# Performance work log

Measured on AMD Instinct MI355X. Metric: run time of the kernel, lower is better.

Reference implementation:

```python
import jax, jax.numpy as jnp
import numpy as np

B, HW, N = 32, 4096, 16
E, KV, FFN = 256, 256, 1024
NUM_ITER = 3
EPS_LN = 1e-5
EPS_ATTN = 1e-5


def _ln(x, g, b):
    m = x.mean(-1, keepdims=True)
    v = ((x - m) ** 2).mean(-1, keepdims=True)
    return (x - m) / jnp.sqrt(v + EPS_LN) * g + b


def _gru_cell(x, h, w_ih, w_hh, b_ih, b_hh):
    # PyTorch GRUCell semantics; gate order r, z, n
    gi = x @ w_ih.T + b_ih
    gh = h @ w_hh.T + b_hh
    ir, iz, inn = jnp.split(gi, 3, axis=-1)
    hr, hz, hn = jnp.split(gh, 3, axis=-1)
    r = jax.nn.sigmoid(ir + hr)
    z = jax.nn.sigmoid(iz + hz)
    n = jnp.tanh(inn + r * hn)
    return (1.0 - z) * n + z * h


def setup_inputs() -> dict:
    key = jax.random.key(0)
    ks = jax.random.split(key, 16)
    s = 0.02
    return {
        "input": jax.random.normal(ks[0], (B, HW, KV), jnp.float32),
        "query": jax.random.normal(ks[1], (B, N, E), jnp.float32),
        "g_kv": jnp.ones((KV,), jnp.float32),
        "b_kv": jnp.zeros((KV,), jnp.float32),
        "w_k": jax.random.normal(ks[2], (E, KV), jnp.float32) * s,
        "w_v": jax.random.normal(ks[3], (E, KV), jnp.float32) * s,
        "g_q": jnp.ones((E,), jnp.float32),
        "b_q": jnp.zeros((E,), jnp.float32),
        "w_q": jax.random.normal(ks[4], (E, E), jnp.float32) * s,
        "w_ih": jax.random.normal(ks[5], (3 * E, E), jnp.float32) * s,
        "w_hh": jax.random.normal(ks[6], (3 * E, E), jnp.float32) * s,
        "b_ih": jnp.zeros((3 * E,), jnp.float32),
        "b_hh": jnp.zeros((3 * E,), jnp.float32),
        "g_2": jnp.ones((E,), jnp.float32),
        "b_2": jnp.zeros((E,), jnp.float32),
        "w_f1": jax.random.normal(ks[7], (FFN, E), jnp.float32) * s,
        "b_f1": jnp.zeros((FFN,), jnp.float32),
        "w_f2": jax.random.normal(ks[8], (E, FFN), jnp.float32) * s,
        "b_f2": jnp.zeros((E,), jnp.float32),
    }


def reference(input, query, g_kv, b_kv, w_k, w_v, g_q, b_q, w_q,
              w_ih, w_hh, b_ih, b_hh, g_2, b_2, w_f1, b_f1, w_f2, b_f2):
    b, n, e = query.shape
    kv = _ln(input, g_kv, b_kv)              # (b, hw, kv)
    k = kv @ w_k.T                           # (b, hw, e)
    v = kv @ w_v.T                           # (b, hw, e)
    scale = e ** (-0.5)

    q = query
    attn = None
    for i in range(NUM_ITER):
        if i + 1 == NUM_ITER:  # bi-level truncated backprop
            q = jax.lax.stop_gradient(q) + query - jax.lax.stop_gradient(query)
        slots_prev = q
        qn = _ln(q, g_q, b_q)
        qp = (qn @ w_q.T) * scale            # (b, n, e)
        logit = jnp.einsum("bqc,bkc->bqk", qp, k)
        attn = jax.nn.softmax(logit, axis=1)           # softmax over slots (inverted)
        attn_w = attn / (attn.sum(2, keepdims=True) + EPS_ATTN)
        updates = jnp.einsum("bqk,bkc->bqc", attn_w, v)
        slots = _gru_cell(updates.reshape(b * n, e), slots_prev.reshape(b * n, e),
                          w_ih, w_hh, b_ih, b_hh).reshape(b, n, e)
        h = jax.nn.gelu(_ln(slots, g_2, b_2) @ w_f1.T + b_f1)
        q = slots + h @ w_f2.T + b_f2
    return q, attn
```

## Files before the change

kernel.cpp:

```cpp
#include <hip/hip_runtime.h>
#include <math.h>

#define NB 32
#define HW 4096
#define NS 16
#define EDIM 256
#define FFND 1024
#define EPS_LN 1e-5f
#define EPS_ATTN 1e-5f
#define BPB 32
#define RPB 128
#define TROWS 16

__device__ __forceinline__ float sigmoidf_(float x) { return 1.0f / (1.0f + __expf(-x)); }
__device__ __forceinline__ float gelu_(float x) {
    float x3 = x * x * x;
    return 0.5f * x * (1.0f + tanhf(0.7978845608028654f * (x + 0.044715f * x3)));
}

__global__ void k_prep(const float* __restrict__ w_q, const float* __restrict__ w_k,
                       float* __restrict__ W) {
    const int j = blockIdx.x;
    const int c = threadIdx.x;
    float acc = 0.f;
    for (int e = 0; e < EDIM; ++e)
        acc += w_q[e * EDIM + j] * w_k[e * EDIM + c];
    W[j * EDIM + c] = acc * 0.0625f;
}

__global__ __launch_bounds__(256) void k_tr(const float* __restrict__ src,
                                            float* __restrict__ dst, int R, int C) {
    __shared__ float tile[64][65];
    const int tilesC = C >> 6;
    const int tR = (blockIdx.x / tilesC) << 6;
    const int tC = (blockIdx.x % tilesC) << 6;
    const int t = threadIdx.x;
    {
        const int r = t >> 2;
        const int c0 = (t & 3) << 4;
#pragma unroll
        for (int i = 0; i < 16; i += 4) {
            const float4 v = *reinterpret_cast<const float4*>(src + (size_t)(tR + r) * C + tC + c0 + i);
            tile[r][c0 + i] = v.x; tile[r][c0 + i + 1] = v.y;
            tile[r][c0 + i + 2] = v.z; tile[r][c0 + i + 3] = v.w;
        }
    }
    __syncthreads();
    {
        const int c = t >> 2;
        const int r0 = (t & 3) << 4;
#pragma unroll
        for (int i = 0; i < 16; ++i)
            dst[(size_t)(tC + c) * R + tR + r0 + i] = tile[r0 + i][c];
    }
}

__global__ void k_qproj(const float* __restrict__ qsrc, const float* __restrict__ g_q,
                        const float* __restrict__ b_q, const float* __restrict__ W,
                        const float* __restrict__ g_kv, const float* __restrict__ b_kv,
                        float* __restrict__ qpk, float* __restrict__ gqbq) {
    const int row = blockIdx.x;
    const int t = threadIdx.x;
    __shared__ float qn[EDIM];
    __shared__ float red[16];
    const float v = qsrc[(size_t)row * EDIM + t];
    float s = v, ss = v * v;
#pragma unroll
    for (int m = 1; m < 64; m <<= 1) { s += __shfl_xor(s, m); ss += __shfl_xor(ss, m); }
    const int wave = t >> 6, lane = t & 63;
    if (lane == 0) { red[wave] = s; red[8 + wave] = ss; }
    __syncthreads();
    const float st = red[0] + red[1] + red[2] + red[3];
    const float sst = red[8] + red[9] + red[10] + red[11];
    const float mean = st * (1.0f / EDIM);
    const float rstd = rsqrtf(sst * (1.0f / EDIM) - mean * mean + EPS_LN);
    qn[t] = (v - mean) * rstd * g_q[t] + b_q[t];
    __syncthreads();
    float acc = 0.f;
    for (int j = 0; j < EDIM; ++j)
        acc += qn[j] * W[j * EDIM + t];
    qpk[(size_t)row * EDIM + t] = acc;
    float u = acc * g_kv[t];
    float w2 = acc * b_kv[t];
#pragma unroll
    for (int m = 1; m < 64; m <<= 1) { u += __shfl_xor(u, m); w2 += __shfl_xor(w2, m); }
    __syncthreads();
    if (lane == 0) { red[wave] = u; red[8 + wave] = w2; }
    __syncthreads();
    if (t == 0) {
        const int b = row >> 4, sl = row & 15;
        gqbq[b * 32 + sl] = red[0] + red[1] + red[2] + red[3];
        gqbq[b * 32 + 16 + sl] = red[8] + red[9] + red[10] + red[11];
    }
}

template <bool LAST>
__global__ __launch_bounds__(256, 2) void k_bigpass(
    const float* __restrict__ input, const float* __restrict__ qpk,
    const float* __restrict__ gqbq, const float* __restrict__ g_kv,
    float* __restrict__ pacc, float* __restrict__ psum, float* __restrict__ attn_out) {
    const int b = blockIdx.x >> 5;
    const int sub = blockIdx.x & 31;
    const int t = threadIdx.x;
    const int w = t >> 6;
    const int lane = t & 63;
    const int g = t >> 4;
    const int j = t & 15;

    __shared__ __align__(16) float G[NS][EDIM];
    __shared__ __align__(16) float stage[TROWS][264];
    __shared__ __align__(16) float wrec[TROWS][20];
    __shared__ float gqbq_s[2][NS];

#pragma unroll
    for (int i = 0; i < 4; ++i) {
        const int idx = i * 1024 + t * 4;
        const float4 qv = *reinterpret_cast<const float4*>(qpk + (size_t)b * 4096 + idx);
        const float4 gv = *reinterpret_cast<const float4*>(g_kv + (idx & 255));
        *reinterpret_cast<float4*>(&G[0][0] + idx) =
            make_float4(qv.x * gv.x, qv.y * gv.y, qv.z * gv.z, qv.w * gv.w);
    }
    if (t < 32) gqbq_s[t >> 4][t & 15] = gqbq[b * 32 + t];
    __syncthreads();

    float acc[4][4];
    float S[4], A[4];
#pragma unroll
    for (int si = 0; si < 4; ++si) {
        acc[si][0] = acc[si][1] = acc[si][2] = acc[si][3] = 0.f;
        S[si] = 0.f; A[si] = 0.f;
    }

    const int rowbase = sub * RPB;
#pragma unroll 1
    for (int tt = 0; tt < RPB / TROWS; ++tt) {
        const int grow = rowbase + tt * TROWS + g;
        const float* xa = input + ((size_t)b * HW + grow) * EDIM;

        float p[NS];
#pragma unroll
        for (int s = 0; s < NS; ++s) p[s] = 0.f;
        float s1 = 0.f, s2 = 0.f;
#pragma unroll
        for (int c = 0; c < 4; ++c) {
            const int off = (c * 16 + j) * 4;
            const float4 x = *reinterpret_cast<const float4*>(xa + off);
            *reinterpret_cast<float4*>(&stage[g][off]) = x;
            s1 += x.x + x.y + x.z + x.w;
            s2 += x.x * x.x + x.y * x.y + x.z * x.z + x.w * x.w;
#pragma unroll
            for (int s = 0; s < NS; ++s) {
                const float4 gg = *reinterpret_cast<const float4*>(&G[s][off]);
                p[s] += x.x * gg.x + x.y * gg.y + x.z * gg.z + x.w * gg.w;
            }
        }
#pragma unroll
        for (int m = 1; m < 16; m <<= 1) {
            s1 += __shfl_xor(s1, m); s2 += __shfl_xor(s2, m);
#pragma unroll
            for (int s = 0; s < NS; ++s) p[s] += __shfl_xor(p[s], m);
        }
        const float mean = s1 * (1.0f / EDIM);
        const float rstd = rsqrtf(s2 * (1.0f / EDIM) - mean * mean + EPS_LN);
        float mx = -1e30f;
#pragma unroll
        for (int s = 0; s < NS; ++s) {
            p[s] = rstd * (p[s] - mean * gqbq_s[0][s]) + gqbq_s[1][s];
            mx = fmaxf(mx, p[s]);
        }
        float tot = 0.f;
#pragma unroll
        for (int s = 0; s < NS; ++s) { p[s] = __expf(p[s] - mx); tot += p[s]; }
        const float inv = 1.0f / tot;
#pragma unroll
        for (int s = 0; s < NS; ++s) p[s] *= inv;

        if (j == 0) {
#pragma unroll
            for (int sq = 0; sq < 4; ++sq)
                *reinterpret_cast<float4*>(&wrec[g][sq * 4]) =
                    make_float4(p[sq * 4], p[sq * 4 + 1], p[sq * 4 + 2], p[sq * 4 + 3]);
            wrec[g][16] = rstd;
            wrec[g][17] = rstd * mean;
            if (LAST) {
#pragma unroll
                for (int s = 0; s < NS; ++s)
                    attn_out[((size_t)(b * NS + s)) * HW + grow] = p[s];
            }
        }
        __syncthreads();

        {
            const int ch = lane * 4;
            const int sbase = w * 4;
#pragma unroll
            for (int r = 0; r < TROWS; ++r) {
                const float4 xv = *reinterpret_cast<const float4*>(&stage[r][ch]);
                const float4 at = *reinterpret_cast<const float4*>(&wrec[r][sbase]);
                const float rr = wrec[r][16];
                const float rm = wrec[r][17];
                float wg;
                wg = at.x * rr;
                acc[0][0] += wg * xv.x; acc[0][1] += wg * xv.y;
                acc[0][2] += wg * xv.z; acc[0][3] += wg * xv.w;
                S[0] += at.x; A[0] += at.x * rm;
                wg = at.y * rr;
                acc[1][0] += wg * xv.x; acc[1][1] += wg * xv.y;
                acc[1][2] += wg * xv.z; acc[1][3] += wg * xv.w;
                S[1] += at.y; A[1] += at.y * rm;
                wg = at.z * rr;
                acc[2][0] += wg * xv.x; acc[2][1] += wg * xv.y;
                acc[2][2] += wg * xv.z; acc[2][3] += wg * xv.w;
                S[2] += at.z; A[2] += at.z * rm;
                wg = at.w * rr;
                acc[3][0] += wg * xv.x; acc[3][1] += wg * xv.y;
                acc[3][2] += wg * xv.z; acc[3][3] += wg * xv.w;
                S[3] += at.w; A[3] += at.w * rm;
            }
        }
        __syncthreads();
    }

#pragma unroll
    for (int si = 0; si < 4; ++si) {
        *reinterpret_cast<float4*>(
            pacc + ((size_t)blockIdx.x * NS + w * 4 + si) * EDIM + lane * 4) =
            make_float4(acc[si][0], acc[si][1], acc[si][2], acc[si][3]);
    }
    if (lane == 0) {
#pragma unroll
        for (int si = 0; si < 4; ++si) {
            psum[blockIdx.x * 32 + w * 4 + si] = S[si];
            psum[blockIdx.x * 32 + 16 + w * 4 + si] = A[si];
        }
    }
}

__global__ __launch_bounds__(256) void k_upd(
    const float* __restrict__ pacc, const float* __restrict__ psum,
    const float* __restrict__ g_kv, const float* __restrict__ b_kv,
    const float* __restrict__ w_vT, float* __restrict__ updates) {
    const int rt = blockIdx.x >> 1;
    const int ct = blockIdx.x & 1;
    const int row0 = rt * 4;
    const int b = row0 >> 4;
    const int s0 = row0 & 15;
    const int t = threadIdx.x;
    __shared__ __align__(16) float ub[4][EDIM];
    __shared__ float sSA[4][2];

    if (t < 8) {
        const int r = t & 3;
        const int isA = t >> 2;
        float v = 0.f;
        for (int p = 0; p < BPB; ++p)
            v += psum[(b * BPB + p) * 32 + isA * 16 + s0 + r];
        sSA[r][isA] = v;
    }
    __syncthreads();
#pragma unroll
    for (int r = 0; r < 4; ++r) {
        float V = 0.f;
        for (int p = 0; p < BPB; ++p)
            V += pacc[((size_t)(b * BPB + p) * NS + s0 + r) * EDIM + t];
        const float Sv = sSA[r][0], Av = sSA[r][1];
        ub[r][t] = (g_kv[t] * (V - Av) + b_kv[t] * Sv) / (Sv + EPS_ATTN);
    }
    __syncthreads();

    const int c = ct * 128 + (t & 127);
    const int half = t >> 7;
    const float* u0 = ub[2 * half];
    const float* u1 = ub[2 * half + 1];
    float a0 = 0.f, a1 = 0.f;
#pragma unroll 4
    for (int j = 0; j < EDIM; j += 4) {
        const float4 x0 = *reinterpret_cast<const float4*>(u0 + j);
        const float4 x1 = *reinterpret_cast<const float4*>(u1 + j);
        const float w0 = w_vT[(size_t)j * EDIM + c];
        const float w1 = w_vT[(size_t)(j + 1) * EDIM + c];
        const float w2 = w_vT[(size_t)(j + 2) * EDIM + c];
        const float w3 = w_vT[(size_t)(j + 3) * EDIM + c];
        a0 += x0.x * w0 + x0.y * w1 + x0.z * w2 + x0.w * w3;
        a1 += x1.x * w0 + x1.y * w1 + x1.z * w2 + x1.w * w3;
    }
    updates[(size_t)(row0 + 2 * half) * EDIM + c] = a0;
    updates[(size_t)(row0 + 2 * half + 1) * EDIM + c] = a1;
}

__global__ __launch_bounds__(256) void k_gates(
    const float* __restrict__ updates, const float* __restrict__ qprev,
    const float* __restrict__ w_ihT, const float* __restrict__ w_hhT,
    const float* __restrict__ b_ih, const float* __restrict__ b_hh,
    float* __restrict__ gig) {
    const int rt = blockIdx.x / 6;
    const int ct = blockIdx.x % 6;
    const int row0 = rt * 4;
    const int t = threadIdx.x;
    const bool ih = ct < 3;
    const int lc = (ih ? ct : ct - 3) * 256 + t;
    const float* __restrict__ src = ih ? updates : qprev;
    const float* __restrict__ wT = ih ? w_ihT : w_hhT;

    __shared__ __align__(16) float in4[4][EDIM];
#pragma unroll
    for (int r = 0; r < 4; ++r)
        in4[r][t] = src[(size_t)(row0 + r) * EDIM + t];
    __syncthreads();

    float a0 = 0.f, a1 = 0.f, a2 = 0.f, a3 = 0.f;
#pragma unroll 4
    for (int j = 0; j < EDIM; j += 4) {
        const float4 x0 = *reinterpret_cast<const float4*>(&in4[0][j]);
        const float4 x1 = *reinterpret_cast<const float4*>(&in4[1][j]);
        const float4 x2 = *reinterpret_cast<const float4*>(&in4[2][j]);
        const float4 x3 = *reinterpret_cast<const float4*>(&in4[3][j]);
        const float w0 = wT[(size_t)j * 768 + lc];
        const float w1 = wT[(size_t)(j + 1) * 768 + lc];
        const float w2 = wT[(size_t)(j + 2) * 768 + lc];
        const float w3 = wT[(size_t)(j + 3) * 768 + lc];
        a0 += x0.x * w0 + x0.y * w1 + x0.z * w2 + x0.w * w3;
        a1 += x1.x * w0 + x1.y * w1 + x1.z * w2 + x1.w * w3;
        a2 += x2.x * w0 + x2.y * w1 + x2.z * w2 + x2.w * w3;
        a3 += x3.x * w0 + x3.y * w1 + x3.z * w2 + x3.w * w3;
    }
    const float bias = ih ? b_ih[lc] : b_hh[lc];
    const int gcol = ih ? lc : 768 + lc;
    gig[(size_t)(row0 + 0) * 1536 + gcol] = a0 + bias;
    gig[(size_t)(row0 + 1) * 1536 + gcol] = a1 + bias;
    gig[(size_t)(row0 + 2) * 1536 + gcol] = a2 + bias;
    gig[(size_t)(row0 + 3) * 1536 + gcol] = a3 + bias;
}

__global__ __launch_bounds__(256) void k_gruffn1(
    const float* __restrict__ gig, const float* __restrict__ qprev,
    const float* __restrict__ g_2, const float* __restrict__ b_2,
    const float* __restrict__ w_f1T, const float* __restrict__ b_f1,
    float* __restrict__ slots, float* __restrict__ h1) {
    const int rt = blockIdx.x >> 2;
    const int ct = blockIdx.x & 3;
    const int row0 = rt * 4;
    const int t = threadIdx.x;
    const int wave = t >> 6, lane = t & 63;
    __shared__ __align__(16) float ln2[4][EDIM];
    __shared__ float red[4][8];

    float sl[4];
#pragma unroll
    for (int r = 0; r < 4; ++r) {
        const size_t base = (size_t)(row0 + r) * 1536;
        const float ir = gig[base + t];
        const float iz = gig[base + 256 + t];
        const float inn = gig[base + 512 + t];
        const float hr = gig[base + 768 + t];
        const float hz = gig[base + 1024 + t];
        const float hn = gig[base + 1280 + t];
        const float h = qprev[(size_t)(row0 + r) * EDIM + t];
        const float rg = sigmoidf_(ir + hr);
        const float z = sigmoidf_(iz + hz);
        const float n = tanhf(inn + rg * hn);
        sl[r] = (1.0f - z) * n + z * h;
    }
    if (ct == 0) {
#pragma unroll
        for (int r = 0; r < 4; ++r)
            slots[(size_t)(row0 + r) * EDIM + t] = sl[r];
    }
    {
        float a[4], qq[4];
#pragma unroll
        for (int r = 0; r < 4; ++r) { a[r] = sl[r]; qq[r] = sl[r] * sl[r]; }
#pragma unroll
        for (int m = 1; m < 64; m <<= 1) {
#pragma unroll
            for (int r = 0; r < 4; ++r) {
                a[r] += __shfl_xor(a[r], m);
                qq[r] += __shfl_xor(qq[r], m);
            }
        }
        if (lane == 0) {
#pragma unroll
            for (int r = 0; r < 4; ++r) { red[wave][r] = a[r]; red[wave][4 + r] = qq[r]; }
        }
    }
    __syncthreads();
    {
        const float g = g_2[t], bb = b_2[t];
#pragma unroll
        for (int r = 0; r < 4; ++r) {
            const float Sv = red[0][r] + red[1][r] + red[2][r] + red[3][r];
            const float Qv = red[0][4 + r] + red[1][4 + r] + red[2][4 + r] + red[3][4 + r];
            const float mn = Sv * (1.0f / EDIM);
            const float rs = rsqrtf(Qv * (1.0f / EDIM) - mn * mn + EPS_LN);
            ln2[r][t] = (sl[r] - mn) * rs * g + bb;
        }
    }
    __syncthreads();

    const int c = ct * 256 + t;
    float a0 = 0.f, a1 = 0.f, a2 = 0.f, a3 = 0.f;
#pragma unroll 4
    for (int j = 0; j < EDIM; j += 4) {
        const float4 x0 = *reinterpret_cast<const float4*>(&ln2[0][j]);
        const float4 x1 = *reinterpret_cast<const float4*>(&ln2[1][j]);
        const float4 x2 = *reinterpret_cast<const float4*>(&ln2[2][j]);
        const float4 x3 = *reinterpret_cast<const float4*>(&ln2[3][j]);
        const float w0 = w_f1T[(size_t)j * FFND + c];
        const float w1 = w_f1T[(size_t)(j + 1) * FFND + c];
        const float w2 = w_f1T[(size_t)(j + 2) * FFND + c];
        const float w3 = w_f1T[(size_t)(j + 3) * FFND + c];
        a0 += x0.x * w0 + x0.y * w1 + x0.z * w2 + x0.w * w3;
        a1 += x1.x * w0 + x1.y * w1 + x1.z * w2 + x1.w * w3;
        a2 += x2.x * w0 + x2.y * w1 + x2.z * w2 + x2.w * w3;
        a3 += x3.x * w0 + x3.y * w1 + x3.z * w2 + x3.w * w3;
    }
    const float bf = b_f1[c];
    h1[(size_t)(row0 + 0) * FFND + c] = gelu_(a0 + bf);
    h1[(size_t)(row0 + 1) * FFND + c] = gelu_(a1 + bf);
    h1[(size_t)(row0 + 2) * FFND + c] = gelu_(a2 + bf);
    h1[(size_t)(row0 + 3) * FFND + c] = gelu_(a3 + bf);
}

__global__ __launch_bounds__(256) void k_ffn2qpk(
    const float* __restrict__ h1, const float* __restrict__ slots,
    const float* __restrict__ w_f2T, const float* __restrict__ b_f2,
    const float* __restrict__ query,
    const float* __restrict__ g_q, const float* __restrict__ b_q,
    const float* __restrict__ W,
    const float* __restrict__ g_kv, const float* __restrict__ b_kv,
    float* __restrict__ q_out, float* __restrict__ qpk, float* __restrict__ gqbq,
    int adjust, int do_qpk) {
    const int row0 = blockIdx.x * 2;
    const int t = threadIdx.x;
    const int wave = t >> 6, lane = t & 63;
    __shared__ __align__(16) float in2[2][FFND];
    __shared__ float red[4][4];
    __shared__ __align__(16) float qn[2][EDIM];

#pragma unroll
    for (int r = 0; r < 2; ++r)
        *reinterpret_cast<float4*>(&in2[r][t * 4]) =
            *reinterpret_cast<const float4*>(h1 + (size_t)(row0 + r) * FFND + t * 4);
    __syncthreads();
    float a0 = 0.f, a1 = 0.f;
#pragma unroll 4
    for (int j = 0; j < FFND; j += 4) {
        const float4 x0 = *reinterpret_cast<const float4*>(&in2[0][j]);
        const float4 x1 = *reinterpret_cast<const float4*>(&in2[1][j]);
        const float w0 = w_f2T[(size_t)j * EDIM + t];
        const float w1 = w_f2T[(size_t)(j + 1) * EDIM + t];
        const float w2 = w_f2T[(size_t)(j + 2) * EDIM + t];
        const float w3 = w_f2T[(size_t)(j + 3) * EDIM + t];
        a0 += x0.x * w0 + x0.y * w1 + x0.z * w2 + x0.w * w3;
        a1 += x1.x * w0 + x1.y * w1 + x1.z * w2 + x1.w * w3;
    }
    const float bf = b_f2[t];
    float v0 = slots[(size_t)row0 * EDIM + t] + a0 + bf;
    float v1 = slots[(size_t)(row0 + 1) * EDIM + t] + a1 + bf;
    if (adjust) {
        const float qq0 = query[(size_t)row0 * EDIM + t];
        const float qq1 = query[(size_t)(row0 + 1) * EDIM + t];
        v0 = (v0 + qq0) - qq0;
        v1 = (v1 + qq1) - qq1;
    }
    q_out[(size_t)row0 * EDIM + t] = v0;
    q_out[(size_t)(row0 + 1) * EDIM + t] = v1;

    if (!do_qpk) return;

    {
        float a0r = v0, q0 = v0 * v0, a1r = v1, q1 = v1 * v1;
#pragma unroll
        for (int m = 1; m < 64; m <<= 1) {
            a0r += __shfl_xor(a0r, m); q0 += __shfl_xor(q0, m);
            a1r += __shfl_xor(a1r, m); q1 += __shfl_xor(q1, m);
        }
        if (lane == 0) { red[wave][0] = a0r; red[wave][1] = q0; red[wave][2] = a1r; red[wave][3] = q1; }
    }
    __syncthreads();
    {
        const float S0 = red[0][0] + red[1][0] + red[2][0] + red[3][0];
        const float Q0 = red[0][1] + red[1][1] + red[2][1] + red[3][1];
        const float S1 = red[0][2] + red[1][2] + red[2][2] + red[3][2];
        const float Q1 = red[0][3] + red[1][3] + red[2][3] + red[3][3];
        const float m0 = S0 * (1.0f / EDIM);
        const float r0 = rsqrtf(Q0 * (1.0f / EDIM) - m0 * m0 + EPS_LN);
        const float m1 = S1 * (1.0f / EDIM);
        const float r1 = rsqrtf(Q1 * (1.0f / EDIM) - m1 * m1 + EPS_LN);
        const float g = g_q[t], bb = b_q[t];
        qn[0][t] = (v0 - m0) * r0 * g + bb;
        qn[1][t] = (v1 - m1) * r1 * g + bb;
    }
    __syncthreads();
    float p0 = 0.f, p1 = 0.f;
#pragma unroll 4
    for (int j = 0; j < EDIM; j += 4) {
        const float4 x0 = *reinterpret_cast<const float4*>(&qn[0][j]);
        const float4 x1 = *reinterpret_cast<const float4*>(&qn[1][j]);
        const float w0 = W[(size_t)j * EDIM + t];
        const float w1 = W[(size_t)(j + 1) * EDIM + t];
        const float w2 = W[(size_t)(j + 2) * EDIM + t];
        const float w3 = W[(size_t)(j + 3) * EDIM + t];
        p0 += x0.x * w0 + x0.y * w1 + x0.z * w2 + x0.w * w3;
        p1 += x1.x * w0 + x1.y * w1 + x1.z * w2 + x1.w * w3;
    }
    qpk[(size_t)row0 * EDIM + t] = p0;
    qpk[(size_t)(row0 + 1) * EDIM + t] = p1;
    {
        const float gk = g_kv[t], bk = b_kv[t];
        float u0 = p0 * gk, w0 = p0 * bk, u1 = p1 * gk, w1 = p1 * bk;
#pragma unroll
        for (int m = 1; m < 64; m <<= 1) {
            u0 += __shfl_xor(u0, m); w0 += __shfl_xor(w0, m);
            u1 += __shfl_xor(u1, m); w1 += __shfl_xor(w1, m);
        }
        __syncthreads();
        if (lane == 0) { red[wave][0] = u0; red[wave][1] = w0; red[wave][2] = u1; red[wave][3] = w1; }
        __syncthreads();
        if (t == 0) {
            const int b = row0 >> 4;
            const int sl = row0 & 15;
            gqbq[b * 32 + sl] = red[0][0] + red[1][0] + red[2][0] + red[3][0];
            gqbq[b * 32 + 16 + sl] = red[0][1] + red[1][1] + red[2][1] + red[3][1];
            gqbq[b * 32 + sl + 1] = red[0][2] + red[1][2] + red[2][2] + red[3][2];
            gqbq[b * 32 + 16 + sl + 1] = red[0][3] + red[1][3] + red[2][3] + red[3][3];
        }
    }
}

extern "C" void kernel_launch(void* const* d_in, const int* in_sizes, int n_in,
                              void* d_out, int out_size, void* d_ws, size_t ws_size,
                              hipStream_t stream) {
    const float* input = (const float*)d_in[0];
    const float* query = (const float*)d_in[1];
    const float* g_kv = (const float*)d_in[2];
    const float* b_kv = (const float*)d_in[3];
    const float* w_k = (const float*)d_in[4];
    const float* w_v = (const float*)d_in[5];
    const float* g_q = (const float*)d_in[6];
    const float* b_q = (const float*)d_in[7];
    const float* w_q = (const float*)d_in[8];
    const float* w_ih = (const float*)d_in[9];
    const float* w_hh = (const float*)d_in[10];
    const float* b_ih = (const float*)d_in[11];
    const float* b_hh = (const float*)d_in[12];
    const float* g_2 = (const float*)d_in[13];
    const float* b_2 = (const float*)d_in[14];
    const float* w_f1 = (const float*)d_in[15];
    const float* b_f1 = (const float*)d_in[16];
    const float* w_f2 = (const float*)d_in[17];
    const float* b_f2 = (const float*)d_in[18];

    float* ws = (float*)d_ws;
    float* W = ws;        ws += 65536;
    float* qpk = ws;      ws += 131072;
    float* gqbq = ws;     ws += 1024;
    float* psum = ws;     ws += 32768;
    float* q_ws = ws;     ws += 131072;
    float* updates = ws;  ws += 131072;
    float* slots = ws;    ws += 131072;
    float* w_vT = ws;     ws += 65536;
    float* w_ihT = ws;    ws += 196608;
    float* w_hhT = ws;    ws += 196608;
    float* w_f1T = ws;    ws += 262144;
    float* w_f2T = ws;    ws += 262144;
    float* pacc = ws;     ws += (size_t)NB * BPB * NS * EDIM;
    float* gig = pacc;
    float* h1 = pacc + 786432;

    float* out_q = (float*)d_out;
    float* out_attn = out_q + (size_t)NB * NS * EDIM;

    k_prep<<<256, 256, 0, stream>>>(w_q, w_k, W);
    k_tr<<<16, 256, 0, stream>>>(w_v, w_vT, 256, 256);
    k_tr<<<48, 256, 0, stream>>>(w_ih, w_ihT, 768, 256);
    k_tr<<<48, 256, 0, stream>>>(w_hh, w_hhT, 768, 256);
    k_tr<<<64, 256, 0, stream>>>(w_f1, w_f1T, 1024, 256);
    k_tr<<<64, 256, 0, stream>>>(w_f2, w_f2T, 256, 1024);
    k_qproj<<<512, 256, 0, stream>>>(query, g_q, b_q, W, g_kv, b_kv, qpk, gqbq);

    const float* qprev[3] = {query, q_ws, q_ws};
    float* qdst[3] = {q_ws, q_ws, out_q};
    const int adj[3] = {0, 1, 0};

    for (int it = 0; it < 3; ++it) {
        const bool last = (it == 2);
        if (last)
            k_bigpass<true><<<NB * BPB, 256, 0, stream>>>(input, qpk, gqbq, g_kv, pacc, psum, out_attn);
        else
            k_bigpass<false><<<NB * BPB, 256, 0, stream>>>(input, qpk, gqbq, g_kv, pacc, psum, nullptr);
        k_upd<<<256, 256, 0, stream>>>(pacc, psum, g_kv, b_kv, w_vT, updates);
        k_gates<<<768, 256, 0, stream>>>(updates, qprev[it], w_ihT, w_hhT, b_ih, b_hh, gig);
        k_gruffn1<<<512, 256, 0, stream>>>(gig, qprev[it], g_2, b_2, w_f1T, b_f1, slots, h1);
        k_ffn2qpk<<<256, 256, 0, stream>>>(h1, slots, w_f2T, b_f2, query, g_q, b_q, W,
                                           g_kv, b_kv, qdst[it], qpk, gqbq,
                                           adj[it], last ? 0 : 1);
    }
}
```

Measured before the change: 543.8 us.

## Prescale qpk by g_kv upstream, read G from global, use DPP row reductions

The kernels that produce qpk now write it already multiplied by g_kv. This lets the big pass drop its shared-memory G staging array and read the 16x256 per-batch slot matrix straight from global memory through the cache. The 16-lane butterfly reductions of the LN statistics and the slot logits are replaced with DPP row_shr adds. This removes one LDS fill and one sync, and uses cheaper cross-lane ops. The risk is that G loads now go through vector memory rather than LDS, which could raise latency in the hot loop. Any other reader of qpk must also expect the pre-scaled values.

```diff
diff --git a/kernel.cpp b/kernel.cpp
--- a/kernel.cpp
+++ b/kernel.cpp
@@ -18,6 +18,19 @@
     return 0.5f * x * (1.0f + tanhf(0.7978845608028654f * (x + 0.044715f * x3)));
 }
 
+__device__ __forceinline__ float rsum16(float v) {
+    int x;
+    x = __builtin_amdgcn_update_dpp(0, __float_as_int(v), 0x128, 0xF, 0xF, true);
+    v += __int_as_float(x);
+    x = __builtin_amdgcn_update_dpp(0, __float_as_int(v), 0x124, 0xF, 0xF, true);
+    v += __int_as_float(x);
+    x = __builtin_amdgcn_update_dpp(0, __float_as_int(v), 0x122, 0xF, 0xF, true);
+    v += __int_as_float(x);
+    x = __builtin_amdgcn_update_dpp(0, __float_as_int(v), 0x121, 0xF, 0xF, true);
+    v += __int_as_float(x);
+    return v;
+}
+
 __global__ void k_prep(const float* __restrict__ w_q, const float* __restrict__ w_k,
                        float* __restrict__ W) {
     const int j = blockIdx.x;
@@ -79,8 +92,9 @@
     float acc = 0.f;
     for (int j = 0; j < EDIM; ++j)
         acc += qn[j] * W[j * EDIM + t];
-    qpk[(size_t)row * EDIM + t] = acc;
-    float u = acc * g_kv[t];
+    const float gk = g_kv[t];
+    qpk[(size_t)row * EDIM + t] = acc * gk;
+    float u = acc * gk;
     float w2 = acc * b_kv[t];
 #pragma unroll
     for (int m = 1; m < 64; m <<= 1) { u += __shfl_xor(u, m); w2 += __shfl_xor(w2, m); }
@@ -107,21 +121,14 @@
     const int g = t >> 4;
     const int j = t & 15;
 
-    __shared__ __align__(16) float G[NS][EDIM];
     __shared__ __align__(16) float stage[TROWS][264];
     __shared__ __align__(16) float wrec[TROWS][20];
     __shared__ float gqbq_s[2][NS];
 
-#pragma unroll
-    for (int i = 0; i < 4; ++i) {
-        const int idx = i * 1024 + t * 4;
-        const float4 qv = *reinterpret_cast<const float4*>(qpk + (size_t)b * 4096 + idx);
-        const float4 gv = *reinterpret_cast<const float4*>(g_kv + (idx & 255));
-        *reinterpret_cast<float4*>(&G[0][0] + idx) =
-            make_float4(qv.x * gv.x, qv.y * gv.y, qv.z * gv.z, qv.w * gv.w);
-    }
     if (t < 32) gqbq_s[t >> 4][t & 15] = gqbq[b * 32 + t];
     __syncthreads();
+
+    const float* __restrict__ Gg = qpk + (size_t)b * 4096;
 
     float acc[4][4];
     float S[4], A[4];
@@ -150,16 +157,15 @@
             s2 += x.x * x.x + x.y * x.y + x.z * x.z + x.w * x.w;
 #pragma unroll
             for (int s = 0; s < NS; ++s) {
-                const float4 gg = *reinterpret_cast<const float4*>(&G[s][off]);
+                const float4 gg = *reinterpret_cast<const float4*>(Gg + s * EDIM + off);
                 p[s] += x.x * gg.x + x.y * gg.y + x.z * gg.z + x.w * gg.w;
             }
         }
-#pragma unroll
-        for (int m = 1; m < 16; m <<= 1) {
-            s1 += __shfl_xor(s1, m); s2 += __shfl_xor(s2, m);
-#pragma unroll
-            for (int s = 0; s < NS; ++s) p[s] += __shfl_xor(p[s], m);
-        }
+        s1 = rsum16(s1);
+        s2 = rsum16(s2);
+#pragma unroll
+        for (int s = 0; s < NS; ++s) p[s] = rsum16(p[s]);
+
         const float mean = s1 * (1.0f / EDIM);
         const float rstd = rsqrtf(s2 * (1.0f / EDIM) - mean * mean + EPS_LN);
         float mx = -1e30f;
@@ -504,10 +510,10 @@
         p0 += x0.x * w0 + x0.y * w1 + x0.z * w2 + x0.w * w3;
         p1 += x1.x * w0 + x1.y * w1 + x1.z * w2 + x1.w * w3;
     }
-    qpk[(size_t)row0 * EDIM + t] = p0;
-    qpk[(size_t)(row0 + 1) * EDIM + t] = p1;
     {
         const float gk = g_kv[t], bk = b_kv[t];
+        qpk[(size_t)row0 * EDIM + t] = p0 * gk;
+        qpk[(size_t)(row0 + 1) * EDIM + t] = p1 * gk;
         float u0 = p0 * gk, w0 = p0 * bk, u1 = p1 * gk, w1 = p1 * bk;
 #pragma unroll
         for (int m = 1; m < 64; m <<= 1) {
```

New measurement: 1.317 ms. 2.42x slower.
